# Optimization experiments

Measured on AMD Instinct MI355X. Metric: run time of the kernel, lower is better.

Reference implementation:

```python
import jax, jax.numpy as jnp
import numpy as np

def setup_inputs() -> dict:
    key = jax.random.key(0)
    ks = jax.random.split(key, 8)
    B, n, in_dim, h = 4, 512, 300, 128
    word_vecs = jax.random.normal(ks[0], (B, n, in_dim), dtype=jnp.float32)
    mask = jnp.zeros((B, n, h), dtype=jnp.float32)
    s_in = 1.0 / np.sqrt(in_dim)
    s_h = 1.0 / np.sqrt(h)
    Wx_w = jax.random.normal(ks[1], (h, in_dim), dtype=jnp.float32) * s_in
    Wx_b = jnp.zeros((h,), dtype=jnp.float32)
    Wa_w = jax.random.normal(ks[2], (h, h), dtype=jnp.float32) * s_h
    Wa_b = jnp.zeros((h,), dtype=jnp.float32)
    Ua_w = jax.random.normal(ks[3], (h, h), dtype=jnp.float32) * s_h
    Ua_b = jnp.zeros((h,), dtype=jnp.float32)
    return {"word_vecs": word_vecs, "mask": mask, "Wx_w": Wx_w, "Wx_b": Wx_b,
            "Wa_w": Wa_w, "Wa_b": Wa_b, "Ua_w": Ua_w, "Ua_b": Ua_b}

def reference(word_vecs, mask, Wx_w, Wx_b, Wa_w, Wa_b, Ua_w, Ua_b):
    # h_vecs: [B, n, h]  (dropout layers are identity in eval mode)
    h_vecs = jnp.tanh(jnp.einsum('bni,hi->bnh', word_vecs, Wx_w) + Wx_b)
    ta = jnp.einsum('bnh,gh->bng', h_vecs, Wa_w) + Wa_b  # [B,n,h]
    tb = jnp.einsum('bnh,gh->bng', h_vecs, Ua_w) + Ua_b  # [B,n,h]
    # additive per-channel scores: [B, q, k, h]
    temp = jax.nn.elu(ta[:, :, None, :] + tb[:, None, :, :])
    a = jax.nn.softmax(temp + mask[:, None, :, :], axis=2)
    # weighted sum over keys: [B, q, h]
    c_vecs = jnp.einsum('bqkh,bkh->bqh', a, h_vecs)
    return c_vecs
```

## Files before the change

### kernel.cpp

```cpp
#include <hip/hip_runtime.h>

#define B_    4
#define N_    512
#define IND_  300
#define H_    128
#define QQ    8
#define KC    16
#define RR    4
#define LOG2E 1.4426950408889634f

__global__ void pack_all(const float* __restrict__ Wx_w,
                         const float* __restrict__ Wa_w,
                         const float* __restrict__ Ua_w,
                         float* __restrict__ WxT4,
                         float* __restrict__ WaT4,
                         float* __restrict__ UaT4) {
    const int blk = blockIdx.x;
    const int t   = threadIdx.x;
    if (blk < IND_) {
        const int i = blk;
        WxT4[(i >> 2) * 512 + t * 4 + (i & 3)] = Wx_w[t * IND_ + i];
    } else if (blk < IND_ + H_) {
        const int i = blk - IND_;
        WaT4[(i >> 2) * 512 + t * 4 + (i & 3)] = Wa_w[t * H_ + i] * LOG2E;
    } else {
        const int i = blk - IND_ - H_;
        UaT4[(i >> 2) * 512 + t * 4 + (i & 3)] = Ua_w[t * H_ + i] * LOG2E;
    }
}

__global__ __launch_bounds__(128) void prep4(
    const float* __restrict__ x,
    const float* __restrict__ WxT4,
    const float* __restrict__ Wx_b,
    const float* __restrict__ WaT4,
    const float* __restrict__ Wa_b,
    const float* __restrict__ UaT4,
    const float* __restrict__ Ua_b,
    const float* __restrict__ mask,
    float* __restrict__ Eta,
    float4* __restrict__ kv)
{
    __shared__ __align__(16) float xs[RR * IND_];
    __shared__ __align__(16) float hs[RR][H_];

    const int r0 = blockIdx.x * RR;
    const int t  = threadIdx.x;

    const float4* xg = (const float4*)(x + (size_t)r0 * IND_);
    float4* xs4 = (float4*)xs;
    #pragma unroll
    for (int i = t; i < RR * IND_ / 4; i += 128) xs4[i] = xg[i];
    __syncthreads();

    float acc[RR];
    {
        const float bx = Wx_b[t];
        #pragma unroll
        for (int r = 0; r < RR; ++r) acc[r] = bx;
    }
    const float4* w4 = (const float4*)WxT4 + t;
    #pragma unroll 5
    for (int i4 = 0; i4 < IND_ / 4; ++i4) {
        float4 w = w4[i4 * 128];
        #pragma unroll
        for (int r = 0; r < RR; ++r) {
            float4 xv = *(const float4*)(xs + r * IND_ + 4 * i4);
            acc[r] = fmaf(w.x, xv.x, acc[r]);
            acc[r] = fmaf(w.y, xv.y, acc[r]);
            acc[r] = fmaf(w.z, xv.z, acc[r]);
            acc[r] = fmaf(w.w, xv.w, acc[r]);
        }
    }
    #pragma unroll
    for (int r = 0; r < RR; ++r) hs[r][t] = tanhf(acc[r]);
    __syncthreads();

    float accA[RR], accU[RR];
    {
        const float ba = Wa_b[t] * LOG2E;
        const float bu = Ua_b[t] * LOG2E;
        #pragma unroll
        for (int r = 0; r < RR; ++r) { accA[r] = ba; accU[r] = bu; }
    }
    const float4* wa4 = (const float4*)WaT4 + t;
    const float4* ua4 = (const float4*)UaT4 + t;
    #pragma unroll 4
    for (int i4 = 0; i4 < H_ / 4; ++i4) {
        float4 wa = wa4[i4 * 128];
        float4 ua = ua4[i4 * 128];
        #pragma unroll
        for (int r = 0; r < RR; ++r) {
            float4 hv = *(const float4*)(&hs[r][4 * i4]);
            accA[r] = fmaf(wa.x, hv.x, accA[r]);
            accA[r] = fmaf(wa.y, hv.y, accA[r]);
            accA[r] = fmaf(wa.z, hv.z, accA[r]);
            accA[r] = fmaf(wa.w, hv.w, accA[r]);
            accU[r] = fmaf(ua.x, hv.x, accU[r]);
            accU[r] = fmaf(ua.y, hv.y, accU[r]);
            accU[r] = fmaf(ua.z, hv.z, accU[r]);
            accU[r] = fmaf(ua.w, hv.w, accU[r]);
        }
    }
    #pragma unroll
    for (int r = 0; r < RR; ++r) {
        const size_t o = (size_t)(r0 + r) * H_ + t;
        Eta[o]  = __builtin_amdgcn_exp2f(accA[r]);
        float M = __builtin_amdgcn_exp2f(mask[o] * LOG2E);
        float h = hs[r][t];
        kv[o]   = make_float4(__builtin_amdgcn_exp2f(accU[r]), M, M * h, 0.f);
    }
}

__global__ __launch_bounds__(128) void attn4(
    const float* __restrict__ Eta,
    const float4* __restrict__ kv,
    float2* __restrict__ accum)
{
    const int c  = blockIdx.x;
    const int qg = blockIdx.y;
    const int b  = blockIdx.z;
    const int h  = threadIdx.x;
    const int q0 = qg * QQ;
    const int k0 = c * (N_ / KC);

    float eta[QQ], l[QQ], cc[QQ];
    #pragma unroll
    for (int j = 0; j < QQ; ++j) {
        eta[j] = Eta[((size_t)(b * N_ + q0 + j)) * H_ + h];
        l[j] = 0.f;
        cc[j] = 0.f;
    }

    const float4* kp = kv + ((size_t)(b * N_ + k0)) * H_ + h;

    #pragma unroll 4
    for (int k = 0; k < N_ / KC; ++k) {
        float4 v = kp[(size_t)k * H_];
        #pragma unroll
        for (int j = 0; j < QQ; ++j) {
            float e  = eta[j] * v.x;
            float pn = __builtin_amdgcn_exp2f(fmaf(e, LOG2E, -LOG2E));
            float p0 = (e > 1.f) ? e : pn;
            l[j]  = fmaf(p0, v.y, l[j]);
            cc[j] = fmaf(p0, v.z, cc[j]);
        }
    }

    #pragma unroll
    for (int j = 0; j < QQ; ++j) {
        accum[((size_t)c * (B_ * N_) + b * N_ + q0 + j) * H_ + h] =
            make_float2(l[j], cc[j]);
    }
}

__global__ void fin4(const float2* __restrict__ accum, float* __restrict__ out) {
    const int idx = blockIdx.x * 256 + threadIdx.x;
    float L = 0.f, C = 0.f;
    #pragma unroll
    for (int c = 0; c < KC; ++c) {
        float2 a = accum[(size_t)c * (B_ * N_ * H_) + idx];
        L += a.x;
        C += a.y;
    }
    out[idx] = C / L;
}

extern "C" void kernel_launch(void* const* d_in, const int* in_sizes, int n_in,
                              void* d_out, int out_size, void* d_ws, size_t ws_size,
                              hipStream_t stream) {
    const float* word_vecs = (const float*)d_in[0];
    const float* mask      = (const float*)d_in[1];
    const float* Wx_w      = (const float*)d_in[2];
    const float* Wx_b      = (const float*)d_in[3];
    const float* Wa_w      = (const float*)d_in[4];
    const float* Wa_b      = (const float*)d_in[5];
    const float* Ua_w      = (const float*)d_in[6];
    const float* Ua_b      = (const float*)d_in[7];
    float* out = (float*)d_out;

    char* p = (char*)d_ws;
    float*  WxT4  = (float*)p;   p += (size_t)75 * 512 * 4;
    float*  WaT4  = (float*)p;   p += (size_t)32 * 512 * 4;
    float*  UaT4  = (float*)p;   p += (size_t)32 * 512 * 4;
    float*  Eta   = (float*)p;   p += (size_t)B_ * N_ * H_ * 4;
    float4* kv    = (float4*)p;  p += (size_t)B_ * N_ * H_ * 16;
    float2* accum = (float2*)p;  p += (size_t)KC * B_ * N_ * H_ * 8;

    pack_all<<<IND_ + 2 * H_, 128, 0, stream>>>(Wx_w, Wa_w, Ua_w, WxT4, WaT4, UaT4);

    prep4<<<(B_ * N_) / RR, 128, 0, stream>>>(word_vecs, WxT4, Wx_b,
                                              WaT4, Wa_b, UaT4, Ua_b,
                                              mask, Eta, kv);

    dim3 grid(KC, N_ / QQ, B_);
    attn4<<<grid, 128, 0, stream>>>(Eta, kv, accum);

    fin4<<<(B_ * N_ * H_) / 256, 256, 0, stream>>>(accum, out);
}
```

Before: 136.8 us.

## Fuse final reduction into attention kernel via atomic counters and pack math

Removes the separate fin4 kernel. Each attention block now bumps a per-(batch, query-group) atomic counter, and the last of the KC chunk blocks sums all partial accumulators and writes the output. The inner loop is also rewritten with 2-wide float vector types so the compiler can emit packed FMA/multiply instructions. The trade is one fewer kernel launch against threadfences, atomics and a serialized tail reduction done by the last block of each group. The counters are zeroed in pack_all on every call.

```diff
diff --git a/kernel.cpp b/kernel.cpp
--- a/kernel.cpp
+++ b/kernel.cpp
@@ -9,14 +9,21 @@
 #define RR    4
 #define LOG2E 1.4426950408889634f
 
+typedef float v2f __attribute__((ext_vector_type(2)));
+
 __global__ void pack_all(const float* __restrict__ Wx_w,
                          const float* __restrict__ Wa_w,
                          const float* __restrict__ Ua_w,
                          float* __restrict__ WxT4,
                          float* __restrict__ WaT4,
-                         float* __restrict__ UaT4) {
+                         float* __restrict__ UaT4,
+                         unsigned int* __restrict__ cnt) {
     const int blk = blockIdx.x;
     const int t   = threadIdx.x;
+    if (blk == 0) {
+        cnt[t] = 0u;
+        cnt[t + 128] = 0u;
+    }
     if (blk < IND_) {
         const int i = blk;
         WxT4[(i >> 2) * 512 + t * 4 + (i & 3)] = Wx_w[t * IND_ + i];
@@ -112,58 +119,78 @@
     }
 }
 
-__global__ __launch_bounds__(128) void attn4(
+__global__ __launch_bounds__(128) void attn5(
     const float* __restrict__ Eta,
     const float4* __restrict__ kv,
-    float2* __restrict__ accum)
+    float2* __restrict__ accum,
+    unsigned int* __restrict__ cnt,
+    float* __restrict__ out)
 {
     const int c  = blockIdx.x;
     const int qg = blockIdx.y;
     const int b  = blockIdx.z;
-    const int h  = threadIdx.x;
+    const int t  = threadIdx.x;
     const int q0 = qg * QQ;
     const int k0 = c * (N_ / KC);
 
-    float eta[QQ], l[QQ], cc[QQ];
-    #pragma unroll
-    for (int j = 0; j < QQ; ++j) {
-        eta[j] = Eta[((size_t)(b * N_ + q0 + j)) * H_ + h];
-        l[j] = 0.f;
-        cc[j] = 0.f;
-    }
-
-    const float4* kp = kv + ((size_t)(b * N_ + k0)) * H_ + h;
+    v2f eta2[QQ / 2];
+    v2f lc[QQ];
+    #pragma unroll
+    for (int j = 0; j < QQ / 2; ++j) {
+        eta2[j].x = Eta[((size_t)(b * N_ + q0 + 2 * j)) * H_ + t];
+        eta2[j].y = Eta[((size_t)(b * N_ + q0 + 2 * j + 1)) * H_ + t];
+    }
+    #pragma unroll
+    for (int j = 0; j < QQ; ++j) lc[j] = (v2f){0.f, 0.f};
+
+    const float4* kp = kv + ((size_t)(b * N_ + k0)) * H_ + t;
 
     #pragma unroll 4
     for (int k = 0; k < N_ / KC; ++k) {
         float4 v = kp[(size_t)k * H_];
+        v2f mm = (v2f){v.y, v.z};
+        #pragma unroll
+        for (int j = 0; j < QQ / 2; ++j) {
+            v2f e2 = eta2[j] * v.x;
+            v2f a2 = e2 * (v2f)(LOG2E) + (v2f)(-LOG2E);
+            float pn0 = __builtin_amdgcn_exp2f(a2.x);
+            float pn1 = __builtin_amdgcn_exp2f(a2.y);
+            float p0 = (e2.x > 1.f) ? e2.x : pn0;
+            float p1 = (e2.y > 1.f) ? e2.y : pn1;
+            lc[2 * j]     += (v2f){p0, p0} * mm;
+            lc[2 * j + 1] += (v2f){p1, p1} * mm;
+        }
+    }
+
+    #pragma unroll
+    for (int j = 0; j < QQ; ++j) {
+        accum[((size_t)c * (B_ * N_) + b * N_ + q0 + j) * H_ + t] =
+            make_float2(lc[j].x, lc[j].y);
+    }
+
+    __threadfence();
+    __shared__ unsigned int last;
+    __syncthreads();
+    if (t == 0) {
+        const int g = b * (N_ / QQ) + qg;
+        last = atomicAdd(&cnt[g], 1u);
+    }
+    __syncthreads();
+    if (last == KC - 1) {
+        __threadfence();
         #pragma unroll
         for (int j = 0; j < QQ; ++j) {
-            float e  = eta[j] * v.x;
-            float pn = __builtin_amdgcn_exp2f(fmaf(e, LOG2E, -LOG2E));
-            float p0 = (e > 1.f) ? e : pn;
-            l[j]  = fmaf(p0, v.y, l[j]);
-            cc[j] = fmaf(p0, v.z, cc[j]);
-        }
-    }
-
-    #pragma unroll
-    for (int j = 0; j < QQ; ++j) {
-        accum[((size_t)c * (B_ * N_) + b * N_ + q0 + j) * H_ + h] =
-            make_float2(l[j], cc[j]);
-    }
-}
-
-__global__ void fin4(const float2* __restrict__ accum, float* __restrict__ out) {
-    const int idx = blockIdx.x * 256 + threadIdx.x;
-    float L = 0.f, C = 0.f;
-    #pragma unroll
-    for (int c = 0; c < KC; ++c) {
-        float2 a = accum[(size_t)c * (B_ * N_ * H_) + idx];
-        L += a.x;
-        C += a.y;
-    }
-    out[idx] = C / L;
+            const size_t o = ((size_t)(b * N_ + q0 + j)) * H_ + t;
+            float L = 0.f, C = 0.f;
+            #pragma unroll
+            for (int cc2 = 0; cc2 < KC; ++cc2) {
+                float2 a = accum[(size_t)cc2 * (B_ * N_ * H_) + o];
+                L += a.x;
+                C += a.y;
+            }
+            out[o] = C / L;
+        }
+    }
 }
 
 extern "C" void kernel_launch(void* const* d_in, const int* in_sizes, int n_in,
@@ -186,15 +213,15 @@
     float*  Eta   = (float*)p;   p += (size_t)B_ * N_ * H_ * 4;
     float4* kv    = (float4*)p;  p += (size_t)B_ * N_ * H_ * 16;
     float2* accum = (float2*)p;  p += (size_t)KC * B_ * N_ * H_ * 8;
-
-    pack_all<<<IND_ + 2 * H_, 128, 0, stream>>>(Wx_w, Wa_w, Ua_w, WxT4, WaT4, UaT4);
+    unsigned int* cnt = (unsigned int*)p;  p += 256 * sizeof(unsigned int);
+
+    pack_all<<<IND_ + 2 * H_, 128, 0, stream>>>(Wx_w, Wa_w, Ua_w,
+                                                WxT4, WaT4, UaT4, cnt);
 
     prep4<<<(B_ * N_) / RR, 128, 0, stream>>>(word_vecs, WxT4, Wx_b,
                                               WaT4, Wa_b, UaT4, Ua_b,
                                               mask, Eta, kv);
 
     dim3 grid(KC, N_ / QQ, B_);
-    attn4<<<grid, 128, 0, stream>>>(Eta, kv, accum);
-
-    fin4<<<(B_ * N_ * H_) / 256, 256, 0, stream>>>(accum, out);
-}
+    attn5<<<grid, 128, 0, stream>>>(Eta, kv, accum, cnt, out);
+}
```

Measured after the change: 452.2 us. +230.6%, slower.
